# Kernel optimization log

Hardware: AMD Instinct MI355X
Metric: run time of the kernel (lower is better)

The kernel has to match this reference:

```python
import jax, jax.numpy as jnp
import numpy as np

N_LAYERS = 4
B, L, D = 2, 2048, 512
H, E = 8, 64          # n_heads = d_model // d_head
DFF = 1024
EPS = 1e-6
MAX_LOG_SCALE = float(np.log(100.0))   # QKNorm max_scale clamp
LOG10 = float(np.log(10.0))            # QKNorm scale init


def rms_norm(x, scale, eps=EPS):
    # matches torch rms_norm: x * (scale * rsqrt(mean(x^2, -1) + eps))
    ms = jnp.mean(jnp.square(x), axis=-1, keepdims=True)
    return x * (scale * jax.lax.rsqrt(ms + eps))


def rope(x):
    # standard rotary embedding over head dim, half-split convention. x: [n,h,l,e]
    e, l = x.shape[-1], x.shape[-2]
    inv = 1.0 / (10000.0 ** (jnp.arange(0, e, 2, dtype=jnp.float32) / e))
    freqs = jnp.arange(l, dtype=jnp.float32)[:, None] * inv[None, :]   # [l, e/2]
    cos, sin = jnp.cos(freqs), jnp.sin(freqs)
    x1, x2 = x[..., : e // 2], x[..., e // 2:]
    return jnp.concatenate([x1 * cos - x2 * sin, x1 * sin + x2 * cos], axis=-1)


def setup_inputs() -> dict:
    key = jax.random.key(0)
    ks = jax.random.split(key, 10)
    s = 0.02
    return {
        "x": jax.random.normal(ks[0], (B, L, D), jnp.float32),
        "cond": jax.random.normal(ks[1], (B, D), jnp.float32),
        "attn_mask": jnp.ones((B, L), jnp.int32),
        # per-layer stacked params (torch Linear(in,out,bias=False) stored as [in,out], y = x @ W)
        "wn_attn": s * jax.random.normal(ks[2], (N_LAYERS, D, D), jnp.float32),      # AdaRMSNorm cond proj (attn)
        "wqkv": s * jax.random.normal(ks[3], (N_LAYERS, D, 3 * D), jnp.float32),
        "qk_scale": jnp.full((N_LAYERS, H), LOG10, jnp.float32),                     # QKNorm per-head log-scale
        "wout": s * jax.random.normal(ks[4], (N_LAYERS, D, D), jnp.float32),
        "wn_ff": s * jax.random.normal(ks[5], (N_LAYERS, D, D), jnp.float32),        # AdaRMSNorm cond proj (ff)
        "wup": s * jax.random.normal(ks[6], (N_LAYERS, D, 2 * DFF), jnp.float32),
        "wdown": s * jax.random.normal(ks[7], (N_LAYERS, DFF, D), jnp.float32),
        "out_scale": jnp.ones((D,), jnp.float32),                                    # final RMSNorm scale
    }


def forward(x, cond, attn_mask, wn_attn, wqkv, qk_scale, wout, wn_ff, wup, wdown, out_scale):
    n, l, d = x.shape
    # mask bias: (attn_mask != 1) * -1e9, repeated 'n l -> n h l s' (query-dim mask, as in source)
    bias = (attn_mask != 1).astype(x.dtype) * -1e9
    bias = bias[:, None, :, None]  # [n,1,l,1] broadcast over heads and key dim

    def block(h_x, p):
        wn_a, w_qkv, qs, w_o, wn_f, w_up, w_dn = p
        # --- self attention ---
        skip = h_x
        y = rms_norm(h_x, (cond @ wn_a + 1.0)[:, None, :])            # AdaRMSNorm
        qkv = y @ w_qkv                                               # [n,l,3d]
        q, k, v = jnp.split(qkv, 3, axis=-1)
        to_heads = lambda t: t.reshape(n, l, H, E).transpose(0, 2, 1, 3)
        q, k, v = to_heads(q), to_heads(k), to_heads(v)
        qs_c = jnp.minimum(qs, MAX_LOG_SCALE)
        hs = jnp.exp(0.5 * qs_c - 0.25 * np.log(E))[:, None, None]    # [H,1,1] QKNorm scale
        q = rope(rms_norm(q, hs))
        k = rope(rms_norm(k, hs))
        scores = jnp.einsum('nhle,nhse->nhls', q, k) / np.sqrt(E) + bias
        attn = jax.nn.softmax(scores, axis=-1)
        o = jnp.einsum('nhls,nhse->nhle', attn, v)
        o = o.transpose(0, 2, 1, 3).reshape(n, l, d)
        h_x = skip + o @ w_o
        # --- GEGLU feed-forward ---
        skip = h_x
        y = rms_norm(h_x, (cond @ wn_f + 1.0)[:, None, :])
        u = y @ w_up
        a, b = jnp.split(u, 2, axis=-1)
        y = a * jax.nn.gelu(b, approximate=False)                     # F.gelu exact
        h_x = skip + y @ w_dn
        return h_x, None

    x, _ = jax.lax.scan(block, x, (wn_attn, wqkv, qk_scale, wout, wn_ff, wup, wdown))
    return rms_norm(x, out_scale)


def reference(x, cond, attn_mask, wn_attn, wqkv, qk_scale, wout, wn_ff, wup, wdown, out_scale):
    return forward(x, cond, attn_mask, wn_attn, wqkv, qk_scale, wout, wn_ff, wup, wdown, out_scale)
```

## Files before the change

### kernel.cpp

```cpp
#include <hip/hip_runtime.h>
#include <hip/hip_bf16.h>

#define NB 2
#define LL 2048
#define DD 512
#define HH 8
#define EE 64
#define DFF 1024
#define NL 4
#define EPS_F 1e-6f

typedef __bf16 bf16x8 __attribute__((ext_vector_type(8)));
typedef float f32x4 __attribute__((ext_vector_type(4)));

__device__ __forceinline__ unsigned short f2bf(float f) {
    unsigned int u = __float_as_uint(f);
    unsigned int r = (u + 0x7FFFu + ((u >> 16) & 1u)) >> 16;
    return (unsigned short)r;
}
__device__ __forceinline__ unsigned int packbf_t(float a, float b) {
    return (__float_as_uint(a) >> 16) | (__float_as_uint(b) & 0xFFFF0000u);
}
__device__ __forceinline__ void gload16(const void* g, void* l) {
    __builtin_amdgcn_global_load_lds(
        (const __attribute__((address_space(1))) unsigned int*)g,
        (__attribute__((address_space(3))) unsigned int*)l, 16, 0, 0);
}

__global__ void rope_table_kernel(float* __restrict__ cosT, float* __restrict__ sinT) {
    int idx = blockIdx.x * 256 + threadIdx.x;
    if (idx >= LL * 32) return;
    int l = idx >> 5, i = idx & 31;
    float inv = powf(10000.f, -(float)i * (1.f / 32.f));
    float ang = (float)l * inv;
    cosT[idx] = cosf(ang);
    sinT[idx] = sinf(ang);
}

__global__ __launch_bounds__(256) void wcast_all_kernel(const float* __restrict__ wqkv,
                                                        const float* __restrict__ wout,
                                                        const float* __restrict__ wup,
                                                        const float* __restrict__ wdown,
                                                        unsigned short* __restrict__ wt) {
    int bid = blockIdx.x;
    int layer = bid / 2560, rem = bid % 2560;
    const float* W; unsigned short* WT; int K, N, t;
    if (rem < 768)       { W = wqkv  + (size_t)layer * 786432;  WT = wt + (size_t)layer * 786432;            K = 512;  N = 1536; t = rem; }
    else if (rem < 1024) { W = wout  + (size_t)layer * 262144;  WT = wt + 3145728 + (size_t)layer * 262144;  K = 512;  N = 512;  t = rem - 768; }
    else if (rem < 2048) { W = wup   + (size_t)layer * 1048576; WT = wt + 4194304 + (size_t)layer * 1048576; K = 512;  N = 2048; t = rem - 1024; }
    else                 { W = wdown + (size_t)layer * 524288;  WT = wt + 8388608 + (size_t)layer * 524288;  K = 1024; N = 512;  t = rem - 2048; }
    int tn = N / 32;
    int n0 = (t % tn) * 32, k0 = (t / tn) * 32;
    __shared__ float tile[32][33];
    int r = threadIdx.x >> 5, c = threadIdx.x & 31;
#pragma unroll
    for (int i = 0; i < 4; ++i)
        tile[r + 8 * i][c] = W[(size_t)(k0 + r + 8 * i) * N + n0 + c];
    __syncthreads();
#pragma unroll
    for (int i = 0; i < 4; ++i)
        WT[(size_t)(n0 + r + 8 * i) * K + k0 + c] = f2bf(tile[c][r + 8 * i]);
}

__global__ __launch_bounds__(256) void cond_all_kernel(const float* __restrict__ cond,
                                                       const float* __restrict__ wn_attn,
                                                       const float* __restrict__ wn_ff,
                                                       float* __restrict__ s_all) {
    int bid = blockIdx.x;
    int d0 = (bid & 7) * 64;
    int b = (bid >> 3) & 1;
    int which = (bid >> 4) & 1;
    int layer = bid >> 5;
    const float* W = (which ? wn_ff : wn_attn) + (size_t)layer * DD * DD;
    int t = threadIdx.x;
    int d = d0 + (t & 63), kq = t >> 6;
    const float* c = cond + b * DD + kq * 128;
    const float* Wp = W + (size_t)(kq * 128) * DD + d;
    float s = 0.f;
#pragma unroll 8
    for (int j = 0; j < 128; ++j) s = fmaf(c[j], Wp[(size_t)j * DD], s);
    __shared__ float red[4][64];
    red[kq][t & 63] = s;
    __syncthreads();
    if (t < 64) {
        float tot = 1.f + red[0][t] + red[1][t] + red[2][t] + red[3][t];
        s_all[((size_t)(layer * 2 + which) * NB + b) * DD + d0 + t] = tot;
    }
}

__global__ __launch_bounds__(256) void rmsnorm_bf16_kernel(const float* __restrict__ x,
                                                           const float* __restrict__ scale,
                                                           unsigned short* __restrict__ y) {
    int row = blockIdx.x;
    int b = row >> 11;
    int t = threadIdx.x;
    float2 v = ((const float2*)(x + (size_t)row * DD))[t];
    float ss = v.x * v.x + v.y * v.y;
#pragma unroll
    for (int o = 32; o > 0; o >>= 1) ss += __shfl_xor(ss, o);
    __shared__ float red[4];
    if ((t & 63) == 0) red[t >> 6] = ss;
    __syncthreads();
    float tot = red[0] + red[1] + red[2] + red[3];
    float inv = rsqrtf(tot * (1.f / DD) + EPS_F);
    float2 s2 = ((const float2*)(scale + b * DD))[t];
    unsigned int lo = f2bf(v.x * s2.x * inv);
    unsigned int hi = f2bf(v.y * s2.y * inv);
    ((unsigned int*)(y + (size_t)row * DD))[t] = lo | (hi << 16);
}

__global__ __launch_bounds__(256) void rmsnorm_f32_kernel(const float* __restrict__ x,
                                                          const float* __restrict__ scale,
                                                          float* __restrict__ y) {
    int row = blockIdx.x;
    int t = threadIdx.x;
    float2 v = ((const float2*)(x + (size_t)row * DD))[t];
    float ss = v.x * v.x + v.y * v.y;
#pragma unroll
    for (int o = 32; o > 0; o >>= 1) ss += __shfl_xor(ss, o);
    __shared__ float red[4];
    if ((t & 63) == 0) red[t >> 6] = ss;
    __syncthreads();
    float tot = red[0] + red[1] + red[2] + red[3];
    float inv = rsqrtf(tot * (1.f / DD) + EPS_F);
    float2 s2 = ((const float2*)scale)[t];
    float2 o2;
    o2.x = v.x * s2.x * inv;
    o2.y = v.y * s2.y * inv;
    ((float2*)(y + (size_t)row * DD))[t] = o2;
}

template <int BN>
__global__ __launch_bounds__(256) void gemm_bf16_kernel(const unsigned short* __restrict__ A,
                                                        const unsigned short* __restrict__ BT,
                                                        const float* __restrict__ R,
                                                        float* __restrict__ C,
                                                        int M, int N, int K) {
    constexpr int NJ = BN / 32;
    __shared__ __align__(16) unsigned short As[2][128 * 32];
    __shared__ __align__(16) unsigned short Bs[2][BN * 32];
    int tid = threadIdx.x;
    int n0 = blockIdx.x * BN, m0 = blockIdx.y * 128;
    int w = tid >> 6, l = tid & 63;
    int wr = w >> 1, wc = w & 1;
    int kf = 8 * (l >> 4);
    int rf = l & 15;

    auto stage = [&](int buf, int k0) {
#pragma unroll
        for (int u = 0; u < 2; ++u) {
            int c = u * 256 + tid;
            int row = c >> 2, ch = c & 3;
            gload16(A + (size_t)(m0 + row) * K + k0 + ch * 8, &As[buf][c * 8]);
        }
#pragma unroll
        for (int u = 0; u < BN / 64; ++u) {
            int c = u * 256 + tid;
            int row = c >> 2, ch = c & 3;
            gload16(BT + (size_t)(n0 + row) * K + k0 + ch * 8, &Bs[buf][c * 8]);
        }
    };

    f32x4 acc[4][NJ] = {};
    const int nt = K / 32;
    stage(0, 0);
    __syncthreads();

    for (int t = 0; t < nt; ++t) {
        if (t + 1 < nt) stage((t + 1) & 1, (t + 1) * 32);
        int cur = t & 1;
        bf16x8 a[4], b[NJ];
#pragma unroll
        for (int i = 0; i < 4; ++i)
            a[i] = *(const bf16x8*)(&As[cur][(wr * 64 + i * 16 + rf) * 32 + kf]);
#pragma unroll
        for (int j = 0; j < NJ; ++j)
            b[j] = *(const bf16x8*)(&Bs[cur][(wc * (BN / 2) + j * 16 + rf) * 32 + kf]);
#pragma unroll
        for (int i = 0; i < 4; ++i)
#pragma unroll
            for (int j = 0; j < NJ; ++j)
                acc[i][j] = __builtin_amdgcn_mfma_f32_16x16x32_bf16(a[i], b[j], acc[i][j], 0, 0, 0);
        __syncthreads();
    }

    int rl = l >> 4, cl = l & 15;
#pragma unroll
    for (int i = 0; i < 4; ++i)
#pragma unroll
        for (int j = 0; j < NJ; ++j)
#pragma unroll
            for (int r = 0; r < 4; ++r) {
                int row = m0 + wr * 64 + i * 16 + rl * 4 + r;
                int col = n0 + wc * (BN / 2) + j * 16 + cl;
                size_t off = (size_t)row * N + col;
                float v = acc[i][j][r];
                if (R) v += R[off];
                C[off] = v;
            }
}

__global__ __launch_bounds__(256) void gemm_bf16_64_kernel(const unsigned short* __restrict__ A,
                                                           const unsigned short* __restrict__ BT,
                                                           const float* __restrict__ R,
                                                           float* __restrict__ C,
                                                           int M, int N, int K) {
    __shared__ __align__(16) unsigned short As[2][64 * 32];
    __shared__ __align__(16) unsigned short Bs[2][64 * 32];
    int tid = threadIdx.x;
    int logical = (blockIdx.x % 8) * 64 + blockIdx.x / 8;
    int n0 = (logical & 7) * 64, m0 = (logical >> 3) * 64;
    int w = tid >> 6, l = tid & 63;
    int wr = w >> 1, wc = w & 1;
    int kf = 8 * (l >> 4);
    int rf = l & 15;

    auto stage = [&](int buf, int k0) {
        int row = tid >> 2, ch = tid & 3;
        gload16(A + (size_t)(m0 + row) * K + k0 + ch * 8, &As[buf][tid * 8]);
        gload16(BT + (size_t)(n0 + row) * K + k0 + ch * 8, &Bs[buf][tid * 8]);
    };

    f32x4 acc[2][2] = {};
    const int nt = K / 32;
    stage(0, 0);
    __syncthreads();

    for (int t = 0; t < nt; ++t) {
        if (t + 1 < nt) stage((t + 1) & 1, (t + 1) * 32);
        int cur = t & 1;
        bf16x8 a[2], b[2];
#pragma unroll
        for (int i = 0; i < 2; ++i)
            a[i] = *(const bf16x8*)(&As[cur][(wr * 32 + i * 16 + rf) * 32 + kf]);
#pragma unroll
        for (int j = 0; j < 2; ++j)
            b[j] = *(const bf16x8*)(&Bs[cur][(wc * 32 + j * 16 + rf) * 32 + kf]);
#pragma unroll
        for (int i = 0; i < 2; ++i)
#pragma unroll
            for (int j = 0; j < 2; ++j)
                acc[i][j] = __builtin_amdgcn_mfma_f32_16x16x32_bf16(a[i], b[j], acc[i][j], 0, 0, 0);
        __syncthreads();
    }

    int rl = l >> 4, cl = l & 15;
#pragma unroll
    for (int i = 0; i < 2; ++i)
#pragma unroll
        for (int j = 0; j < 2; ++j)
#pragma unroll
            for (int r = 0; r < 4; ++r) {
                int row = m0 + wr * 32 + i * 16 + rl * 4 + r;
                int col = n0 + wc * 32 + j * 16 + cl;
                size_t off = (size_t)row * N + col;
                float v = acc[i][j][r];
                if (R) v += R[off];
                C[off] = v;
            }
}

__global__ __launch_bounds__(256) void gemm_qkv_fused_kernel(const unsigned short* __restrict__ A,
                                                             const unsigned short* __restrict__ BT,
                                                             const float* __restrict__ qs,
                                                             const float* __restrict__ cosT,
                                                             const float* __restrict__ sinT,
                                                             unsigned short* __restrict__ qh,
                                                             unsigned short* __restrict__ kh,
                                                             unsigned short* __restrict__ vt) {
    __shared__ __align__(16) unsigned char smem[128 * 65 * sizeof(float)];
    unsigned short* As = (unsigned short*)smem;
    unsigned short* Bs = (unsigned short*)(smem + 16384);
    float* ex = (float*)smem;
    int tid = threadIdx.x;
    int logical = (blockIdx.x % 8) * 96 + blockIdx.x / 8;
    int ct = logical % 24, m0 = (logical / 24) * 128;
    int n0 = ct * 64;
    int w = tid >> 6, l = tid & 63;
    int wr = w >> 1, wc = w & 1;
    int kf = 8 * (l >> 4);
    int rf = l & 15;

    auto stage = [&](int buf, int k0) {
#pragma unroll
        for (int u = 0; u < 2; ++u) {
            int c = u * 256 + tid;
            int row = c >> 2, ch = c & 3;
            gload16(A + (size_t)(m0 + row) * DD + k0 + ch * 8, &As[buf * 4096 + c * 8]);
        }
        int c = tid;
        int row = c >> 2, ch = c & 3;
        gload16(BT + (size_t)(n0 + row) * DD + k0 + ch * 8, &Bs[buf * 2048 + c * 8]);
    };

    f32x4 acc[4][2] = {};
    stage(0, 0);
    __syncthreads();
    for (int t = 0; t < 16; ++t) {
        if (t + 1 < 16) stage((t + 1) & 1, (t + 1) * 32);
        int cur = t & 1;
        bf16x8 a[4], b[2];
#pragma unroll
        for (int i = 0; i < 4; ++i)
            a[i] = *(const bf16x8*)(&As[cur * 4096 + (wr * 64 + i * 16 + rf) * 32 + kf]);
#pragma unroll
        for (int j = 0; j < 2; ++j)
            b[j] = *(const bf16x8*)(&Bs[cur * 2048 + (wc * 32 + j * 16 + rf) * 32 + kf]);
#pragma unroll
        for (int i = 0; i < 4; ++i)
#pragma unroll
            for (int j = 0; j < 2; ++j)
                acc[i][j] = __builtin_amdgcn_mfma_f32_16x16x32_bf16(a[i], b[j], acc[i][j], 0, 0, 0);
        __syncthreads();
    }

    int rl = l >> 4, cl = l & 15;
#pragma unroll
    for (int i = 0; i < 4; ++i)
#pragma unroll
        for (int j = 0; j < 2; ++j)
#pragma unroll
            for (int r = 0; r < 4; ++r)
                ex[(wr * 64 + i * 16 + rl * 4 + r) * 65 + wc * 32 + j * 16 + cl] = acc[i][j][r];
    __syncthreads();

    int b = m0 >> 11;
    int lbase = m0 & (LL - 1);
    if (ct < 16) {
        int h = ct & 7;
        bool isq = ct < 8;
        float hsc = expf(0.5f * fminf(qs[h], 4.60517019f) - 1.03972077f) * 0.35355339059f;
        if (isq) hsc *= 1.44269504f;
        unsigned short* dst = (isq ? qh : kh) + ((size_t)(b * HH + h) * LL) * EE;
#pragma unroll 4
        for (int it = 0; it < 32; ++it) {
            int row = w * 32 + it;
            int lloc = lbase + row;
            float v = ex[row * 65 + l];
            float ss = v * v;
#pragma unroll
            for (int d = 1; d < 64; d <<= 1) ss += __shfl_xor(ss, d);
            float inv = hsc * rsqrtf(ss * (1.f / EE) + EPS_F);
            float pr = ex[row * 65 + (l ^ 32)];
            int i2 = l & 31;
            float c = cosT[lloc * 32 + i2], s = sinT[lloc * 32 + i2];
            float vn = v * inv, pn = pr * inv;
            float o = (l < 32) ? (vn * c - pn * s) : (pn * s + vn * c);
            dst[(size_t)lloc * EE + l] = f2bf(o);
        }
    } else {
        int h = ct - 16;
        int bh = b * HH + h;
#pragma unroll 4
        for (int it = 0; it < 16; ++it) {
            int e = w * 16 + it;
            float v0 = ex[(2 * l) * 65 + e];
            float v1 = ex[(2 * l + 1) * 65 + e];
            unsigned int pk = (unsigned int)f2bf(v0) | ((unsigned int)f2bf(v1) << 16);
            *(unsigned int*)(vt + ((size_t)(bh * EE + e)) * LL + lbase + 2 * l) = pk;
        }
    }
}

__global__ __launch_bounds__(256) void gemm_geglu_kernel(const unsigned short* __restrict__ A,
                                                         const unsigned short* __restrict__ BT,
                                                         unsigned short* __restrict__ G) {
    __shared__ __align__(16) unsigned char smem[128 * 65 * sizeof(float)];
    unsigned short* As = (unsigned short*)smem;
    unsigned short* Bs = (unsigned short*)(smem + 16384);
    float* ep = (float*)smem;
    int tid = threadIdx.x;
    int logical = (blockIdx.x % 8) * 64 + blockIdx.x / 8;
    int n0 = (logical % 16) * 64, m0 = (logical / 16) * 128;
    int w = tid >> 6, l = tid & 63;
    int wr = w >> 1, wc = w & 1;
    int kf = 8 * (l >> 4);
    int rf = l & 15;

    auto stage = [&](int buf, int k0) {
#pragma unroll
        for (int u = 0; u < 2; ++u) {
            int c = u * 256 + tid;
            int row = c >> 2, ch = c & 3;
            gload16(A + (size_t)(m0 + row) * DD + k0 + ch * 8, &As[buf * 4096 + c * 8]);
            int grow = (row < 64) ? (n0 + row) : (DFF + n0 + row - 64);
            gload16(BT + (size_t)grow * DD + k0 + ch * 8, &Bs[buf * 4096 + c * 8]);
        }
    };

    f32x4 acc[4][4] = {};
    stage(0, 0);
    __syncthreads();

    for (int t = 0; t < 16; ++t) {
        if (t + 1 < 16) stage((t + 1) & 1, (t + 1) * 32);
        int cur = t & 1;
        bf16x8 a[4], b[4];
#pragma unroll
        for (int i = 0; i < 4; ++i)
            a[i] = *(const bf16x8*)(&As[cur * 4096 + (wr * 64 + i * 16 + rf) * 32 + kf]);
#pragma unroll
        for (int j = 0; j < 4; ++j)
            b[j] = *(const bf16x8*)(&Bs[cur * 4096 + (wc * 64 + j * 16 + rf) * 32 + kf]);
#pragma unroll
        for (int i = 0; i < 4; ++i)
#pragma unroll
            for (int j = 0; j < 4; ++j)
                acc[i][j] = __builtin_amdgcn_mfma_f32_16x16x32_bf16(a[i], b[j], acc[i][j], 0, 0, 0);
        __syncthreads();
    }

    int rl = l >> 4, cl = l & 15;
    if (wc == 0) {
#pragma unroll
        for (int i = 0; i < 4; ++i)
#pragma unroll
            for (int j = 0; j < 4; ++j)
#pragma unroll
                for (int r = 0; r < 4; ++r)
                    ep[(wr * 64 + i * 16 + rl * 4 + r) * 65 + j * 16 + cl] = acc[i][j][r];
    }
    __syncthreads();
    if (wc == 1) {
#pragma unroll
        for (int i = 0; i < 4; ++i)
#pragma unroll
            for (int j = 0; j < 4; ++j)
#pragma unroll
                for (int r = 0; r < 4; ++r) {
                    int row = wr * 64 + i * 16 + rl * 4 + r;
                    float bv = acc[i][j][r];
                    float av = ep[row * 65 + j * 16 + cl];
                    float ge = 0.5f * bv * (1.f + erff(bv * 0.70710678f));
                    G[(size_t)(m0 + row) * DFF + n0 + j * 16 + cl] = f2bf(av * ge);
                }
    }
}

#define KVB 32
#define KLDP 72
#define VLDP 40
__global__ __launch_bounds__(256) void flash_mfma_kernel(const unsigned short* __restrict__ qh,
                                                         const unsigned short* __restrict__ kh,
                                                         const unsigned short* __restrict__ vt,
                                                         unsigned short* __restrict__ op,
                                                         float* __restrict__ os) {
    __shared__ unsigned short K_lds[2][32 * KLDP];
    __shared__ unsigned short VT_lds[2][64 * VLDP];
    int bid = (blockIdx.x % 8) * 256 + blockIdx.x / 8;
    int qb = bid & 31, h = (bid >> 5) & 7, b = (bid >> 8) & 1, split = bid >> 9;
    int bh = b * HH + h;
    int tid = threadIdx.x, w = tid >> 6, l = tid & 63;
    int lo = l & 15, hi4 = l >> 4;
    int q0 = qb * 64 + w * 16;

    const unsigned short* qbase = qh + ((size_t)bh * LL) * EE;
    bf16x8 qa[2];
#pragma unroll
    for (int s = 0; s < 2; ++s)
        qa[s] = *(const bf16x8*)(qbase + (size_t)(q0 + lo) * EE + s * 32 + 8 * hi4);

    uint4 ov = make_uint4(0x3F803F80u, 0x3F803F80u, 0x3F803F80u, 0x3F803F80u);
    bf16x8 ones = *(bf16x8*)&ov;

    int krow = tid >> 3, kch = tid & 7;
    int vrow = tid >> 2, vch = tid & 3;
    const uint4* gK = (const uint4*)(kh + ((size_t)bh * LL + split * 16 * KVB + krow) * EE + kch * 8);
    const uint4* gV = (const uint4*)(vt + ((size_t)bh * EE + vrow) * LL + split * 16 * KVB + vch * 8);
    const int gKstep = KVB * EE / 8;
    const int gVstep = KVB / 8;
    unsigned short* ldsK = &K_lds[0][krow * KLDP + kch * 8];
    unsigned short* ldsV = &VT_lds[0][vrow * VLDP + vch * 8];
    const int ldsKsz = 32 * KLDP, ldsVsz = 64 * VLDP;

    uint4 pk = *gK, pv = *gV;
    *(uint4*)ldsK = pk;
    *(uint4*)ldsV = pv;
    __syncthreads();

    f32x4 oacc[4] = {};
    f32x4 osum = {};
    const bool lowg = hi4 < 2;
    const bool oddg = hi4 & 1;
    const bool topg = hi4 >> 1;
    const int par = (hi4 ^ (hi4 >> 1)) & 1;

    for (int t = 0; t < 16; ++t) {
        int cur = t & 1;
        if (t + 1 < 16) {
            pk = gK[(t + 1) * gKstep];
            pv = gV[(t + 1) * gVstep];
        }

        const unsigned short* Kc = &K_lds[cur][0];
        const unsigned short* Vc = &VT_lds[cur][0];
        f32x4 S[2] = {};
        __builtin_amdgcn_s_setprio(1);
#pragma unroll
        for (int nf = 0; nf < 2; ++nf)
#pragma unroll
            for (int s = 0; s < 2; ++s) {
                bf16x8 kb = *(const bf16x8*)&Kc[(nf * 16 + lo) * KLDP + s * 32 + 8 * hi4];
                S[nf] = __builtin_amdgcn_mfma_f32_16x16x32_bf16(kb, qa[s], S[nf], 0, 0, 0);
            }
        __builtin_amdgcn_s_setprio(0);

        float p0 = exp2f(S[0][0]), p1 = exp2f(S[0][1]), p2 = exp2f(S[0][2]), p3 = exp2f(S[0][3]);
        float p4 = exp2f(S[1][0]), p5 = exp2f(S[1][1]), p6 = exp2f(S[1][2]), p7 = exp2f(S[1][3]);

        unsigned int u0 = packbf_t(p0, p1), u1 = packbf_t(p2, p3);
        unsigned int u2 = packbf_t(p4, p5), u3 = packbf_t(p6, p7);
        unsigned int keep0 = lowg ? u0 : u2, keep1 = lowg ? u1 : u3;
        unsigned int sA0 = lowg ? u2 : u0, sA1 = lowg ? u3 : u1;
        unsigned int rA0 = __shfl_xor(sA0, 32), rA1 = __shfl_xor(sA1, 32);
        unsigned int sB0 = par ? keep0 : rA0, sB1 = par ? keep1 : rA1;
        unsigned int rB0 = __shfl_xor(sB0, 16), rB1 = __shfl_xor(sB1, 16);
        uint4 paw;
        paw.x = oddg ? rB0 : (topg ? rA0 : keep0);
        paw.y = oddg ? rB1 : (topg ? rA1 : keep1);
        paw.z = oddg ? (topg ? keep0 : rA0) : rB0;
        paw.w = oddg ? (topg ? keep1 : rA1) : rB1;
        bf16x8 pa = *(bf16x8*)&paw;

        __builtin_amdgcn_s_setprio(1);
#pragma unroll
        for (int nf = 0; nf < 4; ++nf) {
            bf16x8 vb = *(const bf16x8*)&Vc[(nf * 16 + lo) * VLDP + 8 * hi4];
            oacc[nf] = __builtin_amdgcn_mfma_f32_16x16x32_bf16(pa, vb, oacc[nf], 0, 0, 0);
        }
        osum = __builtin_amdgcn_mfma_f32_16x16x32_bf16(pa, ones, osum, 0, 0, 0);
        __builtin_amdgcn_s_setprio(0);

        if (t + 1 < 16) {
            *(uint4*)(ldsK + (cur ^ 1) * ldsKsz) = pk;
            *(uint4*)(ldsV + (cur ^ 1) * ldsVsz) = pv;
        }
        __syncthreads();
    }

    unsigned short* opp = op + (size_t)split * (NB * LL * DD);
#pragma unroll
    for (int r = 0; r < 4; ++r) {
        int row = q0 + hi4 * 4 + r;
        unsigned short* optr = opp + ((size_t)(b * LL + row)) * DD + h * EE;
#pragma unroll
        for (int nf = 0; nf < 4; ++nf)
            optr[nf * 16 + lo] = f2bf(oacc[nf][r]);
        if (lo == 0)
            os[split * (NB * HH * LL) + bh * LL + row] = osum[r];
    }
}

__global__ __launch_bounds__(256) void attn_combine_kernel(const unsigned short* __restrict__ op,
                                                           const float* __restrict__ os,
                                                           unsigned short* __restrict__ oh) {
    int idx = (blockIdx.x * 256 + threadIdx.x) * 8;
    int col = idx & 511;
    int h = col >> 6;
    int row = (idx >> 9) & (LL - 1);
    int b = idx >> 20;
    int bh = b * HH + h;
    float s = 0.f;
    float a[8] = {};
#pragma unroll
    for (int sp = 0; sp < 4; ++sp) {
        s += os[sp * (NB * HH * LL) + bh * LL + row];
        uint4 t = *(const uint4*)(op + (size_t)sp * (NB * LL * DD) + idx);
        unsigned int dw[4] = {t.x, t.y, t.z, t.w};
#pragma unroll
        for (int j = 0; j < 4; ++j) {
            a[2 * j]     += __uint_as_float(dw[j] << 16);
            a[2 * j + 1] += __uint_as_float(dw[j] & 0xFFFF0000u);
        }
    }
    float inv = 1.f / s;
    uint4 o4;
    unsigned int* po = (unsigned int*)&o4;
#pragma unroll
    for (int j = 0; j < 4; ++j)
        po[j] = (unsigned int)f2bf(a[2 * j] * inv) | ((unsigned int)f2bf(a[2 * j + 1] * inv) << 16);
    *(uint4*)(oh + idx) = o4;
}

extern "C" void kernel_launch(void* const* d_in, const int* in_sizes, int n_in,
                              void* d_out, int out_size, void* d_ws, size_t ws_size,
                              hipStream_t stream) {
    const float* x        = (const float*)d_in[0];
    const float* cond     = (const float*)d_in[1];
    const float* wn_attn  = (const float*)d_in[3];
    const float* wqkv     = (const float*)d_in[4];
    const float* qk_scale = (const float*)d_in[5];
    const float* wout     = (const float*)d_in[6];
    const float* wn_ff    = (const float*)d_in[7];
    const float* wup      = (const float*)d_in[8];
    const float* wdown    = (const float*)d_in[9];
    const float* out_scale= (const float*)d_in[10];
    float* out = (float*)d_out;

    const int TOK = NB * LL;
    const size_t nHx = (size_t)TOK * DD;
    const size_t M = 1024 * 1024;

    float* ws = (float*)d_ws;
    float* hx  = ws;
    unsigned short* y_bf = (unsigned short*)(ws + 2 * M);
    unsigned short* op   = (unsigned short*)(ws + 3 * M);
    unsigned short* qh_bf = (unsigned short*)(ws + 11 * M);
    unsigned short* g_bf  = (unsigned short*)(ws + 11 * M);
    unsigned short* kh_bf = (unsigned short*)(ws + 12 * M);
    unsigned short* vt_bf = (unsigned short*)(ws + 13 * M);
    unsigned short* oh_bf = (unsigned short*)(ws + 14 * M);
    unsigned short* wt = (unsigned short*)(ws + 15 * M);
    float* smal  = ws + 20 * M;
    float* s_all = smal;
    float* os    = smal + 8192;
    float* cosT  = os + 131072;
    float* sinT  = cosT + 65536;

    hipMemcpyAsync(hx, x, nHx * sizeof(float), hipMemcpyDeviceToDevice, stream);
    rope_table_kernel<<<256, 256, 0, stream>>>(cosT, sinT);
    cond_all_kernel<<<128, 256, 0, stream>>>(cond, wn_attn, wn_ff, s_all);
    wcast_all_kernel<<<10240, 256, 0, stream>>>(wqkv, wout, wup, wdown, wt);

    unsigned short* wqkvT  = wt;
    unsigned short* woutT  = wt + 3145728;
    unsigned short* wupT   = wt + 4194304;
    unsigned short* wdownT = wt + 8388608;

    for (int layer = 0; layer < NL; ++layer) {
        const float* qs = qk_scale + layer * HH;

        rmsnorm_bf16_kernel<<<TOK, 256, 0, stream>>>(hx, s_all + (size_t)(layer * 2 + 0) * NB * DD, y_bf);
        gemm_qkv_fused_kernel<<<768, 256, 0, stream>>>(
            y_bf, wqkvT + (size_t)layer * 786432, qs, cosT, sinT, qh_bf, kh_bf, vt_bf);
        flash_mfma_kernel<<<2048, 256, 0, stream>>>(qh_bf, kh_bf, vt_bf, op, os);
        attn_combine_kernel<<<1024, 256, 0, stream>>>(op, os, oh_bf);
        gemm_bf16_64_kernel<<<512, 256, 0, stream>>>(
            oh_bf, woutT + (size_t)layer * 262144, hx, hx, TOK, 512, 512);

        rmsnorm_bf16_kernel<<<TOK, 256, 0, stream>>>(hx, s_all + (size_t)(layer * 2 + 1) * NB * DD, y_bf);
        gemm_geglu_kernel<<<512, 256, 0, stream>>>(
            y_bf, wupT + (size_t)layer * 1048576, g_bf);
        gemm_bf16_64_kernel<<<512, 256, 0, stream>>>(
            g_bf, wdownT + (size_t)layer * 524288, hx, hx, TOK, 512, 1024);
    }
    rmsnorm_f32_kernel<<<TOK, 256, 0, stream>>>(hx, out_scale, out);
}
```

Before: 525.7 us.

## Fuse split-attention combine into output projection GEMM A-tile loading

Removes the separate attention combine kernel and instead reduces the four split partial outputs and normalizes by their summed softmax denominators while staging the A tile of the wout GEMM. This eliminates one launch per layer and the write/read of the combined bf16 attention output. In exchange, each output-column block re-reads all split partials, multiplying L2 traffic, and the A path becomes register-staged instead of async LDS loads.

```diff
diff --git a/kernel.cpp b/kernel.cpp
--- a/kernel.cpp
+++ b/kernel.cpp
@@ -130,76 +130,6 @@
     ((float2*)(y + (size_t)row * DD))[t] = o2;
 }
 
-template <int BN>
-__global__ __launch_bounds__(256) void gemm_bf16_kernel(const unsigned short* __restrict__ A,
-                                                        const unsigned short* __restrict__ BT,
-                                                        const float* __restrict__ R,
-                                                        float* __restrict__ C,
-                                                        int M, int N, int K) {
-    constexpr int NJ = BN / 32;
-    __shared__ __align__(16) unsigned short As[2][128 * 32];
-    __shared__ __align__(16) unsigned short Bs[2][BN * 32];
-    int tid = threadIdx.x;
-    int n0 = blockIdx.x * BN, m0 = blockIdx.y * 128;
-    int w = tid >> 6, l = tid & 63;
-    int wr = w >> 1, wc = w & 1;
-    int kf = 8 * (l >> 4);
-    int rf = l & 15;
-
-    auto stage = [&](int buf, int k0) {
-#pragma unroll
-        for (int u = 0; u < 2; ++u) {
-            int c = u * 256 + tid;
-            int row = c >> 2, ch = c & 3;
-            gload16(A + (size_t)(m0 + row) * K + k0 + ch * 8, &As[buf][c * 8]);
-        }
-#pragma unroll
-        for (int u = 0; u < BN / 64; ++u) {
-            int c = u * 256 + tid;
-            int row = c >> 2, ch = c & 3;
-            gload16(BT + (size_t)(n0 + row) * K + k0 + ch * 8, &Bs[buf][c * 8]);
-        }
-    };
-
-    f32x4 acc[4][NJ] = {};
-    const int nt = K / 32;
-    stage(0, 0);
-    __syncthreads();
-
-    for (int t = 0; t < nt; ++t) {
-        if (t + 1 < nt) stage((t + 1) & 1, (t + 1) * 32);
-        int cur = t & 1;
-        bf16x8 a[4], b[NJ];
-#pragma unroll
-        for (int i = 0; i < 4; ++i)
-            a[i] = *(const bf16x8*)(&As[cur][(wr * 64 + i * 16 + rf) * 32 + kf]);
-#pragma unroll
-        for (int j = 0; j < NJ; ++j)
-            b[j] = *(const bf16x8*)(&Bs[cur][(wc * (BN / 2) + j * 16 + rf) * 32 + kf]);
-#pragma unroll
-        for (int i = 0; i < 4; ++i)
-#pragma unroll
-            for (int j = 0; j < NJ; ++j)
-                acc[i][j] = __builtin_amdgcn_mfma_f32_16x16x32_bf16(a[i], b[j], acc[i][j], 0, 0, 0);
-        __syncthreads();
-    }
-
-    int rl = l >> 4, cl = l & 15;
-#pragma unroll
-    for (int i = 0; i < 4; ++i)
-#pragma unroll
-        for (int j = 0; j < NJ; ++j)
-#pragma unroll
-            for (int r = 0; r < 4; ++r) {
-                int row = m0 + wr * 64 + i * 16 + rl * 4 + r;
-                int col = n0 + wc * (BN / 2) + j * 16 + cl;
-                size_t off = (size_t)row * N + col;
-                float v = acc[i][j][r];
-                if (R) v += R[off];
-                C[off] = v;
-            }
-}
-
 __global__ __launch_bounds__(256) void gemm_bf16_64_kernel(const unsigned short* __restrict__ A,
                                                            const unsigned short* __restrict__ BT,
                                                            const float* __restrict__ R,
@@ -257,6 +187,102 @@
                 float v = acc[i][j][r];
                 if (R) v += R[off];
                 C[off] = v;
+            }
+}
+
+__global__ __launch_bounds__(256) void gemm_wout_fused_kernel(const unsigned short* __restrict__ op,
+                                                              const float* __restrict__ os,
+                                                              const unsigned short* __restrict__ BT,
+                                                              const float* __restrict__ R,
+                                                              float* __restrict__ C) {
+    __shared__ __align__(16) unsigned short As[2][64 * 32];
+    __shared__ __align__(16) unsigned short Bs[2][64 * 32];
+    int tid = threadIdx.x;
+    int logical = (blockIdx.x % 8) * 64 + blockIdx.x / 8;
+    int n0 = (logical & 7) * 64, m0 = (logical >> 3) * 64;
+    int w = tid >> 6, l = tid & 63;
+    int wr = w >> 1, wc = w & 1;
+    int kf = 8 * (l >> 4);
+    int rf = l & 15;
+
+    int arow = tid >> 2, ach = tid & 3;
+    int token = m0 + arow;
+    int bq = token >> 11, lq = token & (LL - 1);
+    const unsigned short* opb = op + (size_t)token * DD;
+    const float* osb = os + (size_t)(bq * HH) * LL + lq;
+
+    unsigned int tt[4][4];
+    float sinv;
+    auto loadA = [&](int k0) {
+        int col = k0 + ach * 8;
+        int h = col >> 6;
+        float s = 0.f;
+#pragma unroll
+        for (int sp = 0; sp < 4; ++sp) {
+            uint4 t4 = *(const uint4*)(opb + (size_t)sp * (NB * LL * DD) + col);
+            tt[sp][0] = t4.x; tt[sp][1] = t4.y; tt[sp][2] = t4.z; tt[sp][3] = t4.w;
+            s += osb[(size_t)sp * (NB * HH * LL) + h * LL];
+        }
+        sinv = 1.f / s;
+    };
+    auto writeA = [&](int buf) {
+        uint4 o;
+        unsigned int* po = (unsigned int*)&o;
+#pragma unroll
+        for (int d = 0; d < 4; ++d) {
+            float alo = 0.f, ahi = 0.f;
+#pragma unroll
+            for (int sp = 0; sp < 4; ++sp) {
+                alo += __uint_as_float(tt[sp][d] << 16);
+                ahi += __uint_as_float(tt[sp][d] & 0xFFFF0000u);
+            }
+            po[d] = (unsigned int)f2bf(alo * sinv) | ((unsigned int)f2bf(ahi * sinv) << 16);
+        }
+        *(uint4*)&As[buf][tid * 8] = o;
+    };
+    auto stageB = [&](int buf, int k0) {
+        gload16(BT + (size_t)(n0 + (tid >> 2)) * 512 + k0 + (tid & 3) * 8, &Bs[buf][tid * 8]);
+    };
+
+    f32x4 acc[2][2] = {};
+    loadA(0);
+    stageB(0, 0);
+    writeA(0);
+    __syncthreads();
+
+    for (int t = 0; t < 16; ++t) {
+        int cur = t & 1;
+        if (t + 1 < 16) {
+            loadA((t + 1) * 32);
+            stageB(cur ^ 1, (t + 1) * 32);
+        }
+        bf16x8 a[2], b[2];
+#pragma unroll
+        for (int i = 0; i < 2; ++i)
+            a[i] = *(const bf16x8*)(&As[cur][(wr * 32 + i * 16 + rf) * 32 + kf]);
+#pragma unroll
+        for (int j = 0; j < 2; ++j)
+            b[j] = *(const bf16x8*)(&Bs[cur][(wc * 32 + j * 16 + rf) * 32 + kf]);
+#pragma unroll
+        for (int i = 0; i < 2; ++i)
+#pragma unroll
+            for (int j = 0; j < 2; ++j)
+                acc[i][j] = __builtin_amdgcn_mfma_f32_16x16x32_bf16(a[i], b[j], acc[i][j], 0, 0, 0);
+        if (t + 1 < 16) writeA(cur ^ 1);
+        __syncthreads();
+    }
+
+    int rl = l >> 4, cl = l & 15;
+#pragma unroll
+    for (int i = 0; i < 2; ++i)
+#pragma unroll
+        for (int j = 0; j < 2; ++j)
+#pragma unroll
+            for (int r = 0; r < 4; ++r) {
+                int row = m0 + wr * 32 + i * 16 + rl * 4 + r;
+                int col = n0 + wc * 32 + j * 16 + cl;
+                size_t off = (size_t)row * 512 + col;
+                C[off] = acc[i][j][r] + R[off];
             }
 }
 
@@ -551,37 +577,6 @@
     }
 }
 
-__global__ __launch_bounds__(256) void attn_combine_kernel(const unsigned short* __restrict__ op,
-                                                           const float* __restrict__ os,
-                                                           unsigned short* __restrict__ oh) {
-    int idx = (blockIdx.x * 256 + threadIdx.x) * 8;
-    int col = idx & 511;
-    int h = col >> 6;
-    int row = (idx >> 9) & (LL - 1);
-    int b = idx >> 20;
-    int bh = b * HH + h;
-    float s = 0.f;
-    float a[8] = {};
-#pragma unroll
-    for (int sp = 0; sp < 4; ++sp) {
-        s += os[sp * (NB * HH * LL) + bh * LL + row];
-        uint4 t = *(const uint4*)(op + (size_t)sp * (NB * LL * DD) + idx);
-        unsigned int dw[4] = {t.x, t.y, t.z, t.w};
-#pragma unroll
-        for (int j = 0; j < 4; ++j) {
-            a[2 * j]     += __uint_as_float(dw[j] << 16);
-            a[2 * j + 1] += __uint_as_float(dw[j] & 0xFFFF0000u);
-        }
-    }
-    float inv = 1.f / s;
-    uint4 o4;
-    unsigned int* po = (unsigned int*)&o4;
-#pragma unroll
-    for (int j = 0; j < 4; ++j)
-        po[j] = (unsigned int)f2bf(a[2 * j] * inv) | ((unsigned int)f2bf(a[2 * j + 1] * inv) << 16);
-    *(uint4*)(oh + idx) = o4;
-}
-
 extern "C" void kernel_launch(void* const* d_in, const int* in_sizes, int n_in,
                               void* d_out, int out_size, void* d_ws, size_t ws_size,
                               hipStream_t stream) {
@@ -609,7 +604,6 @@
     unsigned short* g_bf  = (unsigned short*)(ws + 11 * M);
     unsigned short* kh_bf = (unsigned short*)(ws + 12 * M);
     unsigned short* vt_bf = (unsigned short*)(ws + 13 * M);
-    unsigned short* oh_bf = (unsigned short*)(ws + 14 * M);
     unsigned short* wt = (unsigned short*)(ws + 15 * M);
     float* smal  = ws + 20 * M;
     float* s_all = smal;
@@ -634,9 +628,8 @@
         gemm_qkv_fused_kernel<<<768, 256, 0, stream>>>(
             y_bf, wqkvT + (size_t)layer * 786432, qs, cosT, sinT, qh_bf, kh_bf, vt_bf);
         flash_mfma_kernel<<<2048, 256, 0, stream>>>(qh_bf, kh_bf, vt_bf, op, os);
-        attn_combine_kernel<<<1024, 256, 0, stream>>>(op, os, oh_bf);
-        gemm_bf16_64_kernel<<<512, 256, 0, stream>>>(
-            oh_bf, woutT + (size_t)layer * 262144, hx, hx, TOK, 512, 512);
+        gemm_wout_fused_kernel<<<512, 256, 0, stream>>>(
+            op, os, woutT + (size_t)layer * 262144, hx, hx);
 
         rmsnorm_bf16_kernel<<<TOK, 256, 0, stream>>>(hx, s_all + (size_t)(layer * 2 + 1) * NB * DD, y_bf);
         gemm_geglu_kernel<<<512, 256, 0, stream>>>(
```

New measurement: 542.4 us. 3.2% more time.
